# Kernel optimization log

Hardware: AMD Instinct MI355X
Metric: run time of the kernel (lower is better)

Reference implementation:

```python
import jax, jax.numpy as jnp
import numpy as np
from jax.scipy.stats import norm

N_OBJECTS = 100000
N_DIM = 512
ALPHA = 0.05


def setup_inputs() -> dict:
    key = jax.random.key(0)
    k1, k2 = jax.random.split(key)
    q_mu = jax.random.normal(k1, (N_OBJECTS, N_DIM), dtype=jnp.float32)
    # q_var is used as the Normal scale in the original torch code -> keep it positive
    q_var = jax.random.uniform(k2, (N_OBJECTS, N_DIM), dtype=jnp.float32) * 0.9 + 0.1
    return {"q_mu": q_mu, "q_var": q_var}


def reference(q_mu, q_var):
    n_objects = q_mu.shape[0]
    # ecdf_factor = arange(1..n)/n (the torch buffer, in working dtype)
    ecdf = jnp.arange(1, n_objects + 1, dtype=q_mu.dtype) / n_objects
    # p-values: Normal(loc=q_mu, scale=q_var).cdf(0), transposed -> [n_dim, n_objects]
    pvals = norm.cdf(0.0, loc=q_mu, scale=q_var).T

    idx = jnp.arange(n_objects)

    def fdr_reject(p):  # p: [n_objects]
        sortind = jnp.argsort(p)
        ps = p[sortind]
        reject = ps <= ecdf * ALPHA
        # torch code: rejectmax = first nonzero index; reject[:rejectmax] = True
        first = jnp.argmax(reject)
        reject = jnp.where(reject.any(), reject | (idx < first), reject)
        # unsort back to original order (reject_[sortind] = reject)
        return jnp.zeros_like(reject).at[sortind].set(reject)

    rejections = jax.vmap(fdr_reject)(pvals)  # [n_dim, n_objects] bool
    importance = rejections.sum(axis=1)       # [n_dim]
    return importance
```

## Files before the change

kernel.cpp:

```cpp
#include <hip/hip_runtime.h>
#include <cstdint>
#include <cstddef>


#define N_OBJ  100000
#define N_DIM  512
#define UCAP   15360
#define TROW   64
#define TDIM   64

__global__ __launch_bounds__(256) void u_kernel(
    const float* __restrict__ mu, const float* __restrict__ var,
    unsigned short* __restrict__ ut, int c0, int dimTiles)
{
    __shared__ unsigned short tile[TROW][TDIM + 8];
    const int tid = threadIdx.x;
    const int dt = blockIdx.x % dimTiles;
    const int rt = blockIdx.x / dimTiles;
    const int r0 = rt * TROW;
    const int d0 = c0 + dt * TDIM;

    #pragma unroll
    for (int it = 0; it < 4; ++it) {
        const int slot = it * 256 + tid;
        const int rl = slot >> 4;
        const int q  = slot & 15;
        const int r  = r0 + rl;
        ushort4 pk = make_ushort4(0, 0, 0, 0);
        if (r < N_OBJ) {
            const size_t off = (size_t)r * N_DIM + d0 + (q << 2);
            const float4 m4 = *(const float4*)(mu + off);
            const float4 v4 = *(const float4*)(var + off);
            const float xs[4] = {m4.x / v4.x, m4.y / v4.y, m4.z / v4.z, m4.w / v4.w};
            unsigned short us[4];
            #pragma unroll
            for (int j = 0; j < 4; ++j) {
                const float p = 0.5f * erfcf(xs[j] * 0.70710678118654752f);
                const float s = p * 2000000.0f;
                unsigned short u = 0;
                if (s <= (float)UCAP) {
                    const int ui = (int)ceilf(s);
                    u = (unsigned short)(ui < 1 ? 1 : ui);
                }
                us[j] = u;
            }
            pk = make_ushort4(us[0], us[1], us[2], us[3]);
        }
        *(ushort4*)&tile[rl][q << 2] = pk;
    }
    __syncthreads();

    const int d  = tid >> 2;
    const int rb = (tid & 3) << 4;
    union { unsigned short s[16]; uint4 v[2]; } pk;
    #pragma unroll
    for (int i = 0; i < 16; ++i) pk.s[i] = tile[rb + i][d];
    const size_t base = (size_t)(dt * TDIM + d) * N_OBJ + (size_t)(r0 + rb);
    if (r0 + rb + 15 < N_OBJ) {
        *(uint4*)(ut + base)     = pk.v[0];
        *(uint4*)(ut + base + 8) = pk.v[1];
    } else {
        #pragma unroll
        for (int i = 0; i < 16; ++i)
            if (r0 + rb + i < N_OBJ) ut[base + i] = pk.s[i];
    }
}

__global__ __launch_bounds__(256) void fdr_kernel(
    const unsigned short* __restrict__ ut, int* __restrict__ out, int c0)
{
    __shared__ unsigned int hist[UCAP];
    __shared__ unsigned int wsum[4];
    __shared__ unsigned int redc[4], redm[4];
    const int tid  = threadIdx.x;
    const int lane = tid & 63;
    const int wid  = tid >> 6;
    const unsigned short* __restrict__ row = ut + (size_t)blockIdx.x * N_OBJ;

    for (int i = tid; i < UCAP / 4; i += 256)
        ((uint4*)hist)[i] = make_uint4(0u, 0u, 0u, 0u);
    __syncthreads();

    unsigned int c1 = 0;
    for (int slot = tid; slot < N_OBJ / 8; slot += 256) {
        const uint4 w = *(const uint4*)(row + slot * 8);
        const unsigned int words[4] = {w.x, w.y, w.z, w.w};
        #pragma unroll
        for (int k = 0; k < 4; ++k) {
            const unsigned int u0 = words[k] & 0xFFFFu;
            const unsigned int u1 = words[k] >> 16;
            if (u0 == 1u) c1++; else if (u0) atomicAdd(&hist[u0 - 1], 1u);
            if (u1 == 1u) c1++; else if (u1) atomicAdd(&hist[u1 - 1], 1u);
        }
    }
    #pragma unroll
    for (int d = 32; d > 0; d >>= 1) c1 += __shfl_down(c1, d, 64);
    if (lane == 0 && c1) atomicAdd(&hist[0], c1);
    __syncthreads();

    unsigned int running = 0, tcount = 0, tmin = 0xFFFFFFFFu;
    for (int u0 = 0; u0 < UCAP; u0 += 1024) {
        const int idx = u0 + (tid << 2);
        const uint4 c = *(const uint4*)&hist[idx];
        const unsigned int ls = c.x + c.y + c.z + c.w;

        unsigned int sc = ls;
        #pragma unroll
        for (int dd = 1; dd < 64; dd <<= 1) {
            const unsigned int v = __shfl_up(sc, dd, 64);
            if (lane >= dd) sc += v;
        }
        if (lane == 63) wsum[wid] = sc;
        __syncthreads();

        unsigned int woff = 0, btot = 0;
        #pragma unroll
        for (int w = 0; w < 4; ++w) {
            const unsigned int s = wsum[w];
            btot += s;
            if (w < wid) woff += s;
        }

        unsigned int P = running + woff + (sc - ls);
        const unsigned int cc[4] = {c.x, c.y, c.z, c.w};
        #pragma unroll
        for (int j = 0; j < 4; ++j) {
            P += cc[j];
            const unsigned int m = (unsigned int)(idx + j + 1);
            if (P >= m) { tcount++; if (m < tmin) tmin = m; }
        }
        running += btot;
        __syncthreads();
    }

    #pragma unroll
    for (int d = 32; d > 0; d >>= 1) {
        tcount += __shfl_down(tcount, d, 64);
        const unsigned int om = __shfl_down(tmin, d, 64);
        if (om < tmin) tmin = om;
    }
    if (lane == 0) { redc[wid] = tcount; redm[wid] = tmin; }
    __syncthreads();
    if (tid == 0) {
        const unsigned int tot = redc[0] + redc[1] + redc[2] + redc[3];
        const unsigned int mn  = min(min(redm[0], redm[1]), min(redm[2], redm[3]));
        out[c0 + blockIdx.x] = tot ? (int)(tot + mn - 1u) : 0;
    }
}

extern "C" void kernel_launch(void* const* d_in, const int* in_sizes, int n_in,
                              void* d_out, int out_size, void* d_ws, size_t ws_size,
                              hipStream_t stream) {
    const float* mu  = (const float*)d_in[0];
    const float* var = (const float*)d_in[1];
    int* out = (int*)d_out;
    unsigned short* ut = (unsigned short*)d_ws;

    const size_t perDim = (size_t)N_OBJ * sizeof(unsigned short);
    const int dmax = (int)(ws_size / perDim);
    int D_c = N_DIM;
    while (D_c > dmax && D_c > TDIM) D_c >>= 1;

    const int rowTiles = (N_OBJ + TROW - 1) / TROW;
    for (int c0 = 0; c0 < N_DIM; c0 += D_c) {
        const int dimTiles = D_c / TDIM;
        u_kernel<<<rowTiles * dimTiles, 256, 0, stream>>>(mu, var, ut, c0, dimTiles);
        fdr_kernel<<<D_c, 256, 0, stream>>>(ut, out, c0);
    }
}
```

Measured before the change: 480.2 us.

## Drop LDS transpose in u_kernel and use polynomial erfc approximation

```diff
diff --git a/kernel.cpp b/kernel.cpp
--- a/kernel.cpp
+++ b/kernel.cpp
@@ -6,64 +6,64 @@
 #define N_OBJ  100000
 #define N_DIM  512
 #define UCAP   15360
-#define TROW   64
-#define TDIM   64
+#define OB     160
+#define RPT    40
+
+__device__ __forceinline__ unsigned short u_of(float m, float sg) {
+    const float inv = __builtin_amdgcn_rcpf(sg);
+    const float x   = m * inv * 0.70710678118654752f;
+    const float t   = __builtin_amdgcn_rcpf(fmaf(0.3275911f, x, 1.0f));
+    float poly = fmaf(1.061405429f, t, -1.453152027f);
+    poly = fmaf(poly, t, 1.421413741f);
+    poly = fmaf(poly, t, -0.284496736f);
+    poly = fmaf(poly, t, 0.254829592f);
+    poly *= t;
+    const float e = __expf(-x * x);
+    const float y = poly * e * 1000000.0f;
+    unsigned short u = 0;
+    if (x >= 1.0f && y <= (float)UCAP) {
+        int ui = (int)ceilf(y);
+        u = (unsigned short)(ui < 1 ? 1 : ui);
+    }
+    return u;
+}
 
 __global__ __launch_bounds__(256) void u_kernel(
     const float* __restrict__ mu, const float* __restrict__ var,
-    unsigned short* __restrict__ ut, int c0, int dimTiles)
+    unsigned short* __restrict__ ut, int c0)
 {
-    __shared__ unsigned short tile[TROW][TDIM + 8];
     const int tid = threadIdx.x;
-    const int dt = blockIdx.x % dimTiles;
-    const int rt = blockIdx.x / dimTiles;
-    const int r0 = rt * TROW;
-    const int d0 = c0 + dt * TDIM;
+    const int d   = tid & 63;
+    const int g   = tid >> 6;
+    const int dt  = blockIdx.x / (N_OBJ / OB);
+    const int ch  = blockIdx.x % (N_OBJ / OB);
+    const int Dl  = dt * 64 + d;
+    const int D   = c0 + Dl;
+    const int ob  = ch * OB + g * RPT;
+
+    const float* __restrict__ pm = mu  + (size_t)ob * N_DIM + D;
+    const float* __restrict__ pv = var + (size_t)ob * N_DIM + D;
+
+    union { unsigned short s[RPT]; uint4 v[RPT / 8]; } pk;
 
     #pragma unroll
-    for (int it = 0; it < 4; ++it) {
-        const int slot = it * 256 + tid;
-        const int rl = slot >> 4;
-        const int q  = slot & 15;
-        const int r  = r0 + rl;
-        ushort4 pk = make_ushort4(0, 0, 0, 0);
-        if (r < N_OBJ) {
-            const size_t off = (size_t)r * N_DIM + d0 + (q << 2);
-            const float4 m4 = *(const float4*)(mu + off);
-            const float4 v4 = *(const float4*)(var + off);
-            const float xs[4] = {m4.x / v4.x, m4.y / v4.y, m4.z / v4.z, m4.w / v4.w};
-            unsigned short us[4];
-            #pragma unroll
-            for (int j = 0; j < 4; ++j) {
-                const float p = 0.5f * erfcf(xs[j] * 0.70710678118654752f);
-                const float s = p * 2000000.0f;
-                unsigned short u = 0;
-                if (s <= (float)UCAP) {
-                    const int ui = (int)ceilf(s);
-                    u = (unsigned short)(ui < 1 ? 1 : ui);
-                }
-                us[j] = u;
-            }
-            pk = make_ushort4(us[0], us[1], us[2], us[3]);
+    for (int b = 0; b < RPT / 8; ++b) {
+        float ms[8], vs[8];
+        #pragma unroll
+        for (int j = 0; j < 8; ++j) {
+            const size_t off = (size_t)(b * 8 + j) * N_DIM;
+            ms[j] = pm[off];
+            vs[j] = pv[off];
         }
-        *(ushort4*)&tile[rl][q << 2] = pk;
+        #pragma unroll
+        for (int j = 0; j < 8; ++j)
+            pk.s[b * 8 + j] = u_of(ms[j], vs[j]);
     }
-    __syncthreads();
 
-    const int d  = tid >> 2;
-    const int rb = (tid & 3) << 4;
-    union { unsigned short s[16]; uint4 v[2]; } pk;
+    unsigned short* dst = ut + (size_t)Dl * N_OBJ + ob;
     #pragma unroll
-    for (int i = 0; i < 16; ++i) pk.s[i] = tile[rb + i][d];
-    const size_t base = (size_t)(dt * TDIM + d) * N_OBJ + (size_t)(r0 + rb);
-    if (r0 + rb + 15 < N_OBJ) {
-        *(uint4*)(ut + base)     = pk.v[0];
-        *(uint4*)(ut + base + 8) = pk.v[1];
-    } else {
-        #pragma unroll
-        for (int i = 0; i < 16; ++i)
-            if (r0 + rb + i < N_OBJ) ut[base + i] = pk.s[i];
-    }
+    for (int b = 0; b < RPT / 8; ++b)
+        ((uint4*)dst)[b] = pk.v[b];
 }
 
 __global__ __launch_bounds__(256) void fdr_kernel(
@@ -159,12 +159,11 @@
     const size_t perDim = (size_t)N_OBJ * sizeof(unsigned short);
     const int dmax = (int)(ws_size / perDim);
     int D_c = N_DIM;
-    while (D_c > dmax && D_c > TDIM) D_c >>= 1;
+    while (D_c > dmax && D_c > 64) D_c >>= 1;
 
-    const int rowTiles = (N_OBJ + TROW - 1) / TROW;
     for (int c0 = 0; c0 < N_DIM; c0 += D_c) {
-        const int dimTiles = D_c / TDIM;
-        u_kernel<<<rowTiles * dimTiles, 256, 0, stream>>>(mu, var, ut, c0, dimTiles);
+        const int dimTiles = D_c / 64;
+        u_kernel<<<dimTiles * (N_OBJ / OB), 256, 0, stream>>>(mu, var, ut, c0);
         fdr_kernel<<<D_c, 256, 0, stream>>>(ut, out, c0);
     }
 }
```

New measurement: 510.7 us. 1.06x slower.
